# Kernel tuning notes

Measured on AMD Instinct MI355X. Metric: run time of the kernel, lower is better.

## Reference

```python
import jax, jax.numpy as jnp
import numpy as np

BATCH, IN_DIM, H, OUT_DIM = 131072, 1024, 256, 256


def _het_act(z, act_id):
    # Per-column heterogeneous activation: act_id[j] in {0:relu,1:tanh,2:gelu(exact),3:sigmoid}
    return jnp.select(
        [act_id == 0, act_id == 1, act_id == 2],
        [jax.nn.relu(z), jnp.tanh(z), jax.nn.gelu(z, approximate=False)],
        jax.nn.sigmoid(z),
    )


def setup_inputs() -> dict:
    key = jax.random.key(0)
    ks = jax.random.split(key, 7)
    def lin(k, fan_in, fan_out):
        bound = 1.0 / np.sqrt(fan_in)
        kw, kb = jax.random.split(k)
        W = jax.random.uniform(kw, (fan_in, fan_out), jnp.float32, -bound, bound)
        b = jax.random.uniform(kb, (fan_out,), jnp.float32, -bound, bound)
        return W, b
    x = jax.random.normal(ks[0], (BATCH, IN_DIM), jnp.float32)
    W1, b1 = lin(ks[1], IN_DIM, H)
    W2, b2 = lin(ks[2], H, H)
    Wout, bout = lin(ks[3], H, OUT_DIM)
    act_id1 = jnp.arange(H, dtype=jnp.int32) % 4  # relu,tanh,gelu,sigmoid cycle
    act_id2 = jnp.arange(H, dtype=jnp.int32) % 4
    return {"x": x, "W1": W1, "b1": b1, "W2": W2, "b2": b2,
            "Wout": Wout, "bout": bout, "act_id1": act_id1, "act_id2": act_id2}


def reference(x, W1, b1, W2, b2, Wout, bout, act_id1, act_id2):
    # Each original layer is 'H' separate Linear(in,1) ops concatenated -> one fused
    # [in, H] matmul with per-column activation, identical math.
    h1 = _het_act(x @ W1 + b1, act_id1)   # [B, H]
    h2 = _het_act(h1 @ W2 + b2, act_id2)  # [B, H]
    return h2 @ Wout + bout               # [B, OUT_DIM]
```

## Files before the change

### kernel.cpp

```cpp
#include <hip/hip_runtime.h>
#include <hip/hip_bf16.h>


typedef __bf16 bf16;
typedef __bf16 bf16x8 __attribute__((ext_vector_type(8)));
typedef float  f32x4  __attribute__((ext_vector_type(4)));

#define BATCH 131072
#define K1    1024
#define HDIM  256

__device__ __forceinline__ float het_act(float z, int aid) {
    if (aid == 0) return fmaxf(z, 0.0f);
    if (aid == 1) {
        float zc = fminf(fmaxf(z, -20.0f), 20.0f);
        float e = __expf(-2.0f * zc);
        return (1.0f - e) / (1.0f + e);
    }
    if (aid == 2) return 0.5f * z * (1.0f + erff(z * 0.70710678118654752f));
    return 1.0f / (1.0f + __expf(-z));
}

__global__ void prep_w(const float* __restrict__ src, bf16* __restrict__ dst,
                       int total, int kshift, int N) {
    int i = blockIdx.x * blockDim.x + threadIdx.x;
    if (i >= total) return;
    int n = i >> kshift;
    int k = i & ((1 << kshift) - 1);
    dst[i] = (bf16)src[(size_t)k * N + n];
}

#define RMA 128
#define BKA 64
#define ASTR 72
#define HSTR 264

__global__ __launch_bounds__(512, 4) void gemm1_kernel(
    const float* __restrict__ x,
    const bf16*  __restrict__ wt1,
    const float* __restrict__ b1,
    const int*   __restrict__ aid1,
    bf16* __restrict__ h1)
{
    __shared__ __align__(16) char smem[RMA * HSTR * 2];
    bf16 (*as)[ASTR] = (bf16(*)[ASTR])smem;
    bf16 (*ws)[ASTR] = (bf16(*)[ASTR])(smem + RMA * ASTR * 2);
    bf16 (*hout)[HSTR] = (bf16(*)[HSTR])smem;

    const int tid  = threadIdx.x;
    const int lane = tid & 63;
    const int wave = tid >> 6;
    const int rg   = wave >> 2;
    const int slab = wave & 3;
    const int l15  = lane & 15;
    const int quad = lane >> 4;
    const size_t row0 = (size_t)blockIdx.x * RMA;

    const int xr0 = tid >> 3;
    const int xr1 = xr0 + 64;
    const int xq  = tid & 7;
    const int wn0 = tid >> 3;
    const int wq  = tid & 7;

    f32x4 acc[4][4];
    #pragma unroll
    for (int i = 0; i < 4; ++i)
        #pragma unroll
        for (int j = 0; j < 4; ++j)
            acc[i][j] = (f32x4){0.f, 0.f, 0.f, 0.f};

    bf16x8 wcur[4], wnxt[4];
    #pragma unroll
    for (int p = 0; p < 4; ++p)
        wcur[p] = *(const bf16x8*)(wt1 + (size_t)(wn0 + p * 64) * K1 + wq * 8);

    for (int kt = 0; kt < K1 / BKA; ++kt) {
        const int k0 = kt * BKA;
        const float* xp0 = x + (row0 + xr0) * K1 + k0 + xq * 8;
        const float* xp1 = x + (row0 + xr1) * K1 + k0 + xq * 8;
        float4 f0a = *(const float4*)xp0;
        float4 f0b = *(const float4*)(xp0 + 4);
        float4 f1a = *(const float4*)xp1;
        float4 f1b = *(const float4*)(xp1 + 4);
        const int k0n = (kt + 1 < K1 / BKA) ? k0 + BKA : 0;
        #pragma unroll
        for (int p = 0; p < 4; ++p)
            wnxt[p] = *(const bf16x8*)(wt1 + (size_t)(wn0 + p * 64) * K1 + k0n + wq * 8);
        #pragma unroll
        for (int p = 0; p < 4; ++p)
            *(bf16x8*)&ws[wn0 + p * 64][wq * 8] = wcur[p];
        {
            bf16x8 va, vb;
            va[0] = (bf16)f0a.x; va[1] = (bf16)f0a.y; va[2] = (bf16)f0a.z; va[3] = (bf16)f0a.w;
            va[4] = (bf16)f0b.x; va[5] = (bf16)f0b.y; va[6] = (bf16)f0b.z; va[7] = (bf16)f0b.w;
            *(bf16x8*)&as[xr0][xq * 8] = va;
            vb[0] = (bf16)f1a.x; vb[1] = (bf16)f1a.y; vb[2] = (bf16)f1a.z; vb[3] = (bf16)f1a.w;
            vb[4] = (bf16)f1b.x; vb[5] = (bf16)f1b.y; vb[6] = (bf16)f1b.z; vb[7] = (bf16)f1b.w;
            *(bf16x8*)&as[xr1][xq * 8] = vb;
        }
        __syncthreads();
        #pragma unroll
        for (int s = 0; s < 2; ++s) {
            bf16x8 afr[4];
            #pragma unroll
            for (int i = 0; i < 4; ++i)
                afr[i] = *(const bf16x8*)&as[rg * 64 + i * 16 + l15][s * 32 + quad * 8];
            #pragma unroll
            for (int j = 0; j < 4; ++j) {
                bf16x8 bfr = *(const bf16x8*)&ws[slab * 64 + j * 16 + l15][s * 32 + quad * 8];
                #pragma unroll
                for (int i = 0; i < 4; ++i)
                    acc[i][j] = __builtin_amdgcn_mfma_f32_16x16x32_bf16(afr[i], bfr, acc[i][j], 0, 0, 0);
            }
        }
        __syncthreads();
        #pragma unroll
        for (int p = 0; p < 4; ++p) wcur[p] = wnxt[p];
    }

    #pragma unroll
    for (int j = 0; j < 4; ++j) {
        int col = slab * 64 + j * 16 + l15;
        float bias = b1[col];
        int aid = aid1[col];
        #pragma unroll
        for (int i = 0; i < 4; ++i)
            #pragma unroll
            for (int r = 0; r < 4; ++r) {
                int row = rg * 64 + i * 16 + quad * 4 + r;
                hout[row][col] = (bf16)het_act(acc[i][j][r] + bias, aid);
            }
    }
    __syncthreads();
    #pragma unroll
    for (int p = 0; p < 8; ++p) {
        int c = tid + p * 512;
        int r = c >> 5, q = c & 31;
        *(bf16x8*)(h1 + (row0 + r) * HDIM + q * 8) = *(const bf16x8*)&hout[r][q * 8];
    }
}

#define RMB 64
#define BKB 64
#define BSTR 72
#define BHSTR 264

__global__ __launch_bounds__(512, 4) void gemm23_kernel(
    const bf16*  __restrict__ h1,
    const bf16*  __restrict__ wt2,
    const float* __restrict__ b2,
    const bf16*  __restrict__ wt3,
    const float* __restrict__ bout,
    const int*   __restrict__ aid2,
    float* __restrict__ out)
{
    __shared__ __align__(16) bf16 hs[RMB][BHSTR];
    __shared__ __align__(16) bf16 ws[HDIM][BSTR];

    const int tid  = threadIdx.x;
    const int lane = tid & 63;
    const int wave = tid >> 6;
    const int rg   = wave >> 2;
    const int slab = wave & 3;
    const int l15  = lane & 15;
    const int quad = lane >> 4;
    const size_t row0 = (size_t)blockIdx.x * RMB;
    const int wn0 = tid >> 3;
    const int wq  = tid & 7;

    bf16x8 hreg[4];
    #pragma unroll
    for (int p = 0; p < 4; ++p) {
        int c = tid + p * 512;
        int r = c >> 5, q = c & 31;
        hreg[p] = *(const bf16x8*)(h1 + (row0 + r) * HDIM + q * 8);
    }
    bf16x8 wcur[4], wnxt[4];
    #pragma unroll
    for (int p = 0; p < 4; ++p)
        wcur[p] = *(const bf16x8*)(wt2 + (size_t)(wn0 + p * 64) * HDIM + wq * 8);
    #pragma unroll
    for (int p = 0; p < 4; ++p) {
        int c = tid + p * 512;
        int r = c >> 5, q = c & 31;
        *(bf16x8*)&hs[r][q * 8] = hreg[p];
    }

    f32x4 acc[2][4];

    #pragma unroll
    for (int i = 0; i < 2; ++i)
        #pragma unroll
        for (int j = 0; j < 4; ++j)
            acc[i][j] = (f32x4){0.f, 0.f, 0.f, 0.f};

    #pragma unroll
    for (int kt = 0; kt < HDIM / BKB; ++kt) {
        const int k0 = kt * BKB;
        #pragma unroll
        for (int p = 0; p < 4; ++p)
            *(bf16x8*)&ws[wn0 + p * 64][wq * 8] = wcur[p];
        const int   k0n  = (kt < 3) ? k0 + BKB : 0;
        const bf16* wsrc = (kt < 3) ? wt2 : wt3;
        #pragma unroll
        for (int p = 0; p < 4; ++p)
            wnxt[p] = *(const bf16x8*)(wsrc + (size_t)(wn0 + p * 64) * HDIM + k0n + wq * 8);
        __syncthreads();
        #pragma unroll
        for (int s = 0; s < 2; ++s) {
            bf16x8 afr[2];
            #pragma unroll
            for (int i = 0; i < 2; ++i)
                afr[i] = *(const bf16x8*)&hs[rg * 32 + i * 16 + l15][k0 + s * 32 + quad * 8];
            #pragma unroll
            for (int j = 0; j < 4; ++j) {
                bf16x8 bfr = *(const bf16x8*)&ws[slab * 64 + j * 16 + l15][s * 32 + quad * 8];
                #pragma unroll
                for (int i = 0; i < 2; ++i)
                    acc[i][j] = __builtin_amdgcn_mfma_f32_16x16x32_bf16(afr[i], bfr, acc[i][j], 0, 0, 0);
            }
        }
        __syncthreads();
        #pragma unroll
        for (int p = 0; p < 4; ++p) wcur[p] = wnxt[p];
    }
    #pragma unroll
    for (int j = 0; j < 4; ++j) {
        int col = slab * 64 + j * 16 + l15;
        float bias = b2[col];
        int aid = aid2[col];
        #pragma unroll
        for (int i = 0; i < 2; ++i)
            #pragma unroll
            for (int r = 0; r < 4; ++r) {
                int row = rg * 32 + i * 16 + quad * 4 + r;
                hs[row][col] = (bf16)het_act(acc[i][j][r] + bias, aid);
            }
    }

    #pragma unroll
    for (int i = 0; i < 2; ++i)
        #pragma unroll
        for (int j = 0; j < 4; ++j)
            acc[i][j] = (f32x4){0.f, 0.f, 0.f, 0.f};

    #pragma unroll
    for (int kt = 0; kt < HDIM / BKB; ++kt) {
        const int k0 = kt * BKB;
        #pragma unroll
        for (int p = 0; p < 4; ++p)
            *(bf16x8*)&ws[wn0 + p * 64][wq * 8] = wcur[p];
        const int k0n = (kt < 3) ? k0 + BKB : 0;
        #pragma unroll
        for (int p = 0; p < 4; ++p)
            wnxt[p] = *(const bf16x8*)(wt3 + (size_t)(wn0 + p * 64) * HDIM + k0n + wq * 8);
        __syncthreads();
        #pragma unroll
        for (int s = 0; s < 2; ++s) {
            bf16x8 afr[2];
            #pragma unroll
            for (int i = 0; i < 2; ++i)
                afr[i] = *(const bf16x8*)&hs[rg * 32 + i * 16 + l15][k0 + s * 32 + quad * 8];
            #pragma unroll
            for (int j = 0; j < 4; ++j) {
                bf16x8 bfr = *(const bf16x8*)&ws[slab * 64 + j * 16 + l15][s * 32 + quad * 8];
                #pragma unroll
                for (int i = 0; i < 2; ++i)
                    acc[i][j] = __builtin_amdgcn_mfma_f32_16x16x32_bf16(afr[i], bfr, acc[i][j], 0, 0, 0);
            }
        }
        __syncthreads();
        #pragma unroll
        for (int p = 0; p < 4; ++p) wcur[p] = wnxt[p];
    }
    #pragma unroll
    for (int j = 0; j < 4; ++j) {
        int col = slab * 64 + j * 16 + l15;
        float bias = bout[col];
        #pragma unroll
        for (int i = 0; i < 2; ++i)
            #pragma unroll
            for (int r = 0; r < 4; ++r) {
                int row = rg * 32 + i * 16 + quad * 4 + r;
                out[(row0 + row) * HDIM + col] = acc[i][j][r] + bias;
            }
    }
}

#define FRM 64
#define FAPAD 40
#define FHPAD 264

__global__ __launch_bounds__(256, 2) void hetnet_fused(
    const float* __restrict__ x, const bf16* __restrict__ wt1, const float* __restrict__ b1,
    const bf16* __restrict__ wt2, const float* __restrict__ b2,
    const bf16* __restrict__ wt3, const float* __restrict__ bout,
    const int* __restrict__ aid1, const int* __restrict__ aid2, float* __restrict__ out)
{
    __shared__ __align__(16) bf16 hs[FRM][FHPAD];
    __shared__ __align__(16) bf16 as[FRM][FAPAD];
    __shared__ __align__(16) bf16 ws[HDIM][FAPAD];

    const int tid = threadIdx.x, lane = tid & 63, wave = tid >> 6;
    const int l15 = lane & 15, quad = lane >> 4;
    const size_t row0 = (size_t)blockIdx.x * FRM;
    f32x4 acc[4][4];

    #pragma unroll
    for (int i = 0; i < 4; ++i)
        #pragma unroll
        for (int j = 0; j < 4; ++j) acc[i][j] = (f32x4){0.f,0.f,0.f,0.f};
    for (int kt = 0; kt < K1 / 32; ++kt) {
        const int k0 = kt * 32;
        { int r = tid >> 2, q = tid & 3;
          const float* xp = x + (row0 + r) * K1 + k0 + q * 8;
          float4 f0 = *(const float4*)xp; float4 f1 = *(const float4*)(xp + 4);
          bf16x8 v; v[0]=(bf16)f0.x; v[1]=(bf16)f0.y; v[2]=(bf16)f0.z; v[3]=(bf16)f0.w;
          v[4]=(bf16)f1.x; v[5]=(bf16)f1.y; v[6]=(bf16)f1.z; v[7]=(bf16)f1.w;
          *(bf16x8*)&as[r][q * 8] = v; }
        #pragma unroll
        for (int p = 0; p < 4; ++p) {
            int c = tid + p * 256, n = c >> 2, q = c & 3;
            *(bf16x8*)&ws[n][q * 8] = *(const bf16x8*)(wt1 + (size_t)n * K1 + k0 + q * 8);
        }
        __syncthreads();
        bf16x8 afr[4];
        #pragma unroll
        for (int i = 0; i < 4; ++i) afr[i] = *(const bf16x8*)&as[i*16 + l15][quad*8];
        #pragma unroll
        for (int j = 0; j < 4; ++j) {
            bf16x8 bfr = *(const bf16x8*)&ws[wave*64 + j*16 + l15][quad*8];
            #pragma unroll
            for (int i = 0; i < 4; ++i)
                acc[i][j] = __builtin_amdgcn_mfma_f32_16x16x32_bf16(afr[i], bfr, acc[i][j], 0,0,0);
        }
        __syncthreads();
    }
    #pragma unroll
    for (int j = 0; j < 4; ++j) {
        int col = wave*64 + j*16 + l15; float bias = b1[col]; int aid = aid1[col];
        #pragma unroll
        for (int i = 0; i < 4; ++i)
            #pragma unroll
            for (int r = 0; r < 4; ++r)
                hs[i*16 + quad*4 + r][col] = (bf16)het_act(acc[i][j][r] + bias, aid);
    }
    const bf16* wts[2] = {wt2, wt3};
    for (int g = 0; g < 2; ++g) {
        #pragma unroll
        for (int i = 0; i < 4; ++i)
            #pragma unroll
            for (int j = 0; j < 4; ++j) acc[i][j] = (f32x4){0.f,0.f,0.f,0.f};
        for (int kt = 0; kt < HDIM / 32; ++kt) {
            const int k0 = kt * 32;
            #pragma unroll
            for (int p = 0; p < 4; ++p) {
                int c = tid + p * 256, n = c >> 2, q = c & 3;
                *(bf16x8*)&ws[n][q * 8] = *(const bf16x8*)(wts[g] + (size_t)n * HDIM + k0 + q * 8);
            }
            __syncthreads();
            bf16x8 afr[4];
            #pragma unroll
            for (int i = 0; i < 4; ++i) afr[i] = *(const bf16x8*)&hs[i*16 + l15][k0 + quad*8];
            #pragma unroll
            for (int j = 0; j < 4; ++j) {
                bf16x8 bfr = *(const bf16x8*)&ws[wave*64 + j*16 + l15][quad*8];
                #pragma unroll
                for (int i = 0; i < 4; ++i)
                    acc[i][j] = __builtin_amdgcn_mfma_f32_16x16x32_bf16(afr[i], bfr, acc[i][j], 0,0,0);
            }
            __syncthreads();
        }
        if (g == 0) {
            #pragma unroll
            for (int j = 0; j < 4; ++j) {
                int col = wave*64 + j*16 + l15; float bias = b2[col]; int aid = aid2[col];
                #pragma unroll
                for (int i = 0; i < 4; ++i)
                    #pragma unroll
                    for (int r = 0; r < 4; ++r)
                        hs[i*16 + quad*4 + r][col] = (bf16)het_act(acc[i][j][r] + bias, aid);
            }
        } else {
            #pragma unroll
            for (int j = 0; j < 4; ++j) {
                int col = wave*64 + j*16 + l15; float bias = bout[col];
                #pragma unroll
                for (int i = 0; i < 4; ++i)
                    #pragma unroll
                    for (int r = 0; r < 4; ++r)
                        out[(row0 + i*16 + quad*4 + r) * HDIM + col] = acc[i][j][r] + bias;
            }
        }
    }
}

extern "C" void kernel_launch(void* const* d_in, const int* in_sizes, int n_in,
                              void* d_out, int out_size, void* d_ws, size_t ws_size,
                              hipStream_t stream) {
    const float* x    = (const float*)d_in[0];
    const float* W1   = (const float*)d_in[1];
    const float* b1   = (const float*)d_in[2];
    const float* W2   = (const float*)d_in[3];
    const float* b2   = (const float*)d_in[4];
    const float* Wout = (const float*)d_in[5];
    const float* bout = (const float*)d_in[6];
    const int*   aid1 = (const int*)d_in[7];
    const int*   aid2 = (const int*)d_in[8];
    float* out = (float*)d_out;

    bf16* wt1 = (bf16*)d_ws;
    bf16* wt2 = wt1 + 256 * 1024;
    bf16* wt3 = wt2 + 256 * 256;
    bf16* h1  = wt3 + 256 * 256;

    const size_t need = (size_t)(256 * 1024 + 2 * 256 * 256) * 2
                      + (size_t)BATCH * HDIM * 2;

    prep_w<<<(K1 * HDIM + 255) / 256, 256, 0, stream>>>(W1, wt1, K1 * HDIM, 10, HDIM);
    prep_w<<<(HDIM * HDIM + 255) / 256, 256, 0, stream>>>(W2, wt2, HDIM * HDIM, 8, HDIM);
    prep_w<<<(HDIM * HDIM + 255) / 256, 256, 0, stream>>>(Wout, wt3, HDIM * HDIM, 8, HDIM);

    if (ws_size >= need) {
        gemm1_kernel<<<BATCH / RMA, 512, 0, stream>>>(x, wt1, b1, aid1, h1);
        gemm23_kernel<<<BATCH / RMB, 512, 0, stream>>>(h1, wt2, b2, wt3, bout, aid2, out);
    } else {
        hetnet_fused<<<BATCH / FRM, 256, 0, stream>>>(x, wt1, b1, wt2, b2, wt3, bout,
                                                      aid1, aid2, out);
    }
}
```

Baseline: 982.2 us.

## Fuse all three layers into one kernel with B-fragments read from global

Measured after the change: 952.1 us. 3.1% less time.

```diff
diff --git a/kernel.cpp b/kernel.cpp
--- a/kernel.cpp
+++ b/kernel.cpp
@@ -30,22 +30,23 @@
     dst[i] = (bf16)src[(size_t)k * N + n];
 }
 
-#define RMA 128
-#define BKA 64
+#define RM   128
 #define ASTR 72
 #define HSTR 264
 
-__global__ __launch_bounds__(512, 4) void gemm1_kernel(
+__global__ __launch_bounds__(512, 4) void hetnet_one(
     const float* __restrict__ x,
     const bf16*  __restrict__ wt1,
-    const float* __restrict__ b1,
-    const int*   __restrict__ aid1,
-    bf16* __restrict__ h1)
+    const float* __restrict__ b1,  const int* __restrict__ aid1,
+    const bf16*  __restrict__ wt2,
+    const float* __restrict__ b2,  const int* __restrict__ aid2,
+    const bf16*  __restrict__ wt3,
+    const float* __restrict__ bout,
+    float* __restrict__ out)
 {
-    __shared__ __align__(16) char smem[RMA * HSTR * 2];
+    __shared__ __align__(16) char smem[RM * HSTR * 2];
     bf16 (*as)[ASTR] = (bf16(*)[ASTR])smem;
-    bf16 (*ws)[ASTR] = (bf16(*)[ASTR])(smem + RMA * ASTR * 2);
-    bf16 (*hout)[HSTR] = (bf16(*)[HSTR])smem;
+    bf16 (*hs)[HSTR] = (bf16(*)[HSTR])smem;
 
     const int tid  = threadIdx.x;
     const int lane = tid & 63;
@@ -54,13 +55,11 @@
     const int slab = wave & 3;
     const int l15  = lane & 15;
     const int quad = lane >> 4;
-    const size_t row0 = (size_t)blockIdx.x * RMA;
-
-    const int xr0 = tid >> 3;
-    const int xr1 = xr0 + 64;
-    const int xq  = tid & 7;
-    const int wn0 = tid >> 3;
-    const int wq  = tid & 7;
+    const size_t row0 = (size_t)blockIdx.x * RM;
+
+    const int xr = tid >> 3;
+    const int xq = tid & 7;
+    const float* xbase = x + (row0 + xr) * K1 + xq * 8;
 
     f32x4 acc[4][4];
     #pragma unroll
@@ -69,329 +68,147 @@
         for (int j = 0; j < 4; ++j)
             acc[i][j] = (f32x4){0.f, 0.f, 0.f, 0.f};
 
-    bf16x8 wcur[4], wnxt[4];
-    #pragma unroll
-    for (int p = 0; p < 4; ++p)
-        wcur[p] = *(const bf16x8*)(wt1 + (size_t)(wn0 + p * 64) * K1 + wq * 8);
-
-    for (int kt = 0; kt < K1 / BKA; ++kt) {
-        const int k0 = kt * BKA;
-        const float* xp0 = x + (row0 + xr0) * K1 + k0 + xq * 8;
-        const float* xp1 = x + (row0 + xr1) * K1 + k0 + xq * 8;
-        float4 f0a = *(const float4*)xp0;
-        float4 f0b = *(const float4*)(xp0 + 4);
-        float4 f1a = *(const float4*)xp1;
-        float4 f1b = *(const float4*)(xp1 + 4);
-        const int k0n = (kt + 1 < K1 / BKA) ? k0 + BKA : 0;
-        #pragma unroll
-        for (int p = 0; p < 4; ++p)
-            wnxt[p] = *(const bf16x8*)(wt1 + (size_t)(wn0 + p * 64) * K1 + k0n + wq * 8);
-        #pragma unroll
-        for (int p = 0; p < 4; ++p)
-            *(bf16x8*)&ws[wn0 + p * 64][wq * 8] = wcur[p];
-        {
-            bf16x8 va, vb;
-            va[0] = (bf16)f0a.x; va[1] = (bf16)f0a.y; va[2] = (bf16)f0a.z; va[3] = (bf16)f0a.w;
-            va[4] = (bf16)f0b.x; va[5] = (bf16)f0b.y; va[6] = (bf16)f0b.z; va[7] = (bf16)f0b.w;
-            *(bf16x8*)&as[xr0][xq * 8] = va;
-            vb[0] = (bf16)f1a.x; vb[1] = (bf16)f1a.y; vb[2] = (bf16)f1a.z; vb[3] = (bf16)f1a.w;
-            vb[4] = (bf16)f1b.x; vb[5] = (bf16)f1b.y; vb[6] = (bf16)f1b.z; vb[7] = (bf16)f1b.w;
-            *(bf16x8*)&as[xr1][xq * 8] = vb;
-        }
-        __syncthreads();
+    {
+        float4 f0 = *(const float4*)(xbase);
+        float4 f1 = *(const float4*)(xbase + 4);
+        float4 f2 = *(const float4*)(xbase + (size_t)64 * K1);
+        float4 f3 = *(const float4*)(xbase + (size_t)64 * K1 + 4);
+        bf16x8 va, vb;
+        va[0]=(bf16)f0.x; va[1]=(bf16)f0.y; va[2]=(bf16)f0.z; va[3]=(bf16)f0.w;
+        va[4]=(bf16)f1.x; va[5]=(bf16)f1.y; va[6]=(bf16)f1.z; va[7]=(bf16)f1.w;
+        vb[0]=(bf16)f2.x; vb[1]=(bf16)f2.y; vb[2]=(bf16)f2.z; vb[3]=(bf16)f2.w;
+        vb[4]=(bf16)f3.x; vb[5]=(bf16)f3.y; vb[6]=(bf16)f3.z; vb[7]=(bf16)f3.w;
+        *(bf16x8*)&as[xr][xq * 8] = va;
+        *(bf16x8*)&as[64 + xr][xq * 8] = vb;
+    }
+    __syncthreads();
+
+    for (int kt = 0; kt < K1 / 64; ++kt) {
+        const int buf  = (kt & 1) * RM;
+        const int nbuf = RM - buf;
+        float4 f0, f1, f2, f3;
+        if (kt < 15) {
+            const float* xp = xbase + (kt + 1) * 64;
+            f0 = *(const float4*)(xp);
+            f1 = *(const float4*)(xp + 4);
+            f2 = *(const float4*)(xp + (size_t)64 * K1);
+            f3 = *(const float4*)(xp + (size_t)64 * K1 + 4);
+        }
         #pragma unroll
         for (int s = 0; s < 2; ++s) {
             bf16x8 afr[4];
             #pragma unroll
             for (int i = 0; i < 4; ++i)
-                afr[i] = *(const bf16x8*)&as[rg * 64 + i * 16 + l15][s * 32 + quad * 8];
+                afr[i] = *(const bf16x8*)&as[buf + rg * 64 + i * 16 + l15][s * 32 + quad * 8];
             #pragma unroll
             for (int j = 0; j < 4; ++j) {
-                bf16x8 bfr = *(const bf16x8*)&ws[slab * 64 + j * 16 + l15][s * 32 + quad * 8];
+                bf16x8 bfr = *(const bf16x8*)(wt1
+                    + (size_t)(slab * 64 + j * 16 + l15) * K1 + kt * 64 + s * 32 + quad * 8);
                 #pragma unroll
                 for (int i = 0; i < 4; ++i)
                     acc[i][j] = __builtin_amdgcn_mfma_f32_16x16x32_bf16(afr[i], bfr, acc[i][j], 0, 0, 0);
             }
         }
+        if (kt < 15) {
+            bf16x8 va, vb;
+            va[0]=(bf16)f0.x; va[1]=(bf16)f0.y; va[2]=(bf16)f0.z; va[3]=(bf16)f0.w;
+            va[4]=(bf16)f1.x; va[5]=(bf16)f1.y; va[6]=(bf16)f1.z; va[7]=(bf16)f1.w;
+            vb[0]=(bf16)f2.x; vb[1]=(bf16)f2.y; vb[2]=(bf16)f2.z; vb[3]=(bf16)f2.w;
+            vb[4]=(bf16)f3.x; vb[5]=(bf16)f3.y; vb[6]=(bf16)f3.z; vb[7]=(bf16)f3.w;
+            *(bf16x8*)&as[nbuf + xr][xq * 8] = va;
+            *(bf16x8*)&as[nbuf + 64 + xr][xq * 8] = vb;
+        }
         __syncthreads();
-        #pragma unroll
-        for (int p = 0; p < 4; ++p) wcur[p] = wnxt[p];
     }
 
     #pragma unroll
     for (int j = 0; j < 4; ++j) {
-        int col = slab * 64 + j * 16 + l15;
-        float bias = b1[col];
-        int aid = aid1[col];
+        const int col = slab * 64 + j * 16 + l15;
+        const float bias = b1[col];
+        const int aid = aid1[col];
         #pragma unroll
         for (int i = 0; i < 4; ++i)
             #pragma unroll
-            for (int r = 0; r < 4; ++r) {
-                int row = rg * 64 + i * 16 + quad * 4 + r;
-                hout[row][col] = (bf16)het_act(acc[i][j][r] + bias, aid);
-            }
-    }
-    __syncthreads();
-    #pragma unroll
-    for (int p = 0; p < 8; ++p) {
-        int c = tid + p * 512;
-        int r = c >> 5, q = c & 31;
-        *(bf16x8*)(h1 + (row0 + r) * HDIM + q * 8) = *(const bf16x8*)&hout[r][q * 8];
-    }
-}
-
-#define RMB 64
-#define BKB 64
-#define BSTR 72
-#define BHSTR 264
-
-__global__ __launch_bounds__(512, 4) void gemm23_kernel(
-    const bf16*  __restrict__ h1,
-    const bf16*  __restrict__ wt2,
-    const float* __restrict__ b2,
-    const bf16*  __restrict__ wt3,
-    const float* __restrict__ bout,
-    const int*   __restrict__ aid2,
-    float* __restrict__ out)
-{
-    __shared__ __align__(16) bf16 hs[RMB][BHSTR];
-    __shared__ __align__(16) bf16 ws[HDIM][BSTR];
-
-    const int tid  = threadIdx.x;
-    const int lane = tid & 63;
-    const int wave = tid >> 6;
-    const int rg   = wave >> 2;
-    const int slab = wave & 3;
-    const int l15  = lane & 15;
-    const int quad = lane >> 4;
-    const size_t row0 = (size_t)blockIdx.x * RMB;
-    const int wn0 = tid >> 3;
-    const int wq  = tid & 7;
-
-    bf16x8 hreg[4];
-    #pragma unroll
-    for (int p = 0; p < 4; ++p) {
-        int c = tid + p * 512;
-        int r = c >> 5, q = c & 31;
-        hreg[p] = *(const bf16x8*)(h1 + (row0 + r) * HDIM + q * 8);
-    }
-    bf16x8 wcur[4], wnxt[4];
-    #pragma unroll
-    for (int p = 0; p < 4; ++p)
-        wcur[p] = *(const bf16x8*)(wt2 + (size_t)(wn0 + p * 64) * HDIM + wq * 8);
-    #pragma unroll
-    for (int p = 0; p < 4; ++p) {
-        int c = tid + p * 512;
-        int r = c >> 5, q = c & 31;
-        *(bf16x8*)&hs[r][q * 8] = hreg[p];
-    }
-
-    f32x4 acc[2][4];
-
-    #pragma unroll
-    for (int i = 0; i < 2; ++i)
+            for (int r = 0; r < 4; ++r)
+                hs[rg * 64 + i * 16 + quad * 4 + r][col] = (bf16)het_act(acc[i][j][r] + bias, aid);
+    }
+    __syncthreads();
+
+    #pragma unroll
+    for (int i = 0; i < 4; ++i)
         #pragma unroll
         for (int j = 0; j < 4; ++j)
             acc[i][j] = (f32x4){0.f, 0.f, 0.f, 0.f};
 
     #pragma unroll
-    for (int kt = 0; kt < HDIM / BKB; ++kt) {
-        const int k0 = kt * BKB;
-        #pragma unroll
-        for (int p = 0; p < 4; ++p)
-            *(bf16x8*)&ws[wn0 + p * 64][wq * 8] = wcur[p];
-        const int   k0n  = (kt < 3) ? k0 + BKB : 0;
-        const bf16* wsrc = (kt < 3) ? wt2 : wt3;
-        #pragma unroll
-        for (int p = 0; p < 4; ++p)
-            wnxt[p] = *(const bf16x8*)(wsrc + (size_t)(wn0 + p * 64) * HDIM + k0n + wq * 8);
-        __syncthreads();
+    for (int kt = 0; kt < HDIM / 64; ++kt) {
         #pragma unroll
         for (int s = 0; s < 2; ++s) {
-            bf16x8 afr[2];
-            #pragma unroll
-            for (int i = 0; i < 2; ++i)
-                afr[i] = *(const bf16x8*)&hs[rg * 32 + i * 16 + l15][k0 + s * 32 + quad * 8];
+            bf16x8 afr[4];
+            #pragma unroll
+            for (int i = 0; i < 4; ++i)
+                afr[i] = *(const bf16x8*)&hs[rg * 64 + i * 16 + l15][kt * 64 + s * 32 + quad * 8];
             #pragma unroll
             for (int j = 0; j < 4; ++j) {
-                bf16x8 bfr = *(const bf16x8*)&ws[slab * 64 + j * 16 + l15][s * 32 + quad * 8];
+                bf16x8 bfr = *(const bf16x8*)(wt2
+                    + (size_t)(slab * 64 + j * 16 + l15) * HDIM + kt * 64 + s * 32 + quad * 8);
                 #pragma unroll
-                for (int i = 0; i < 2; ++i)
+                for (int i = 0; i < 4; ++i)
                     acc[i][j] = __builtin_amdgcn_mfma_f32_16x16x32_bf16(afr[i], bfr, acc[i][j], 0, 0, 0);
             }
         }
-        __syncthreads();
-        #pragma unroll
-        for (int p = 0; p < 4; ++p) wcur[p] = wnxt[p];
-    }
+    }
+    __syncthreads();
+
     #pragma unroll
     for (int j = 0; j < 4; ++j) {
-        int col = slab * 64 + j * 16 + l15;
-        float bias = b2[col];
-        int aid = aid2[col];
-        #pragma unroll
-        for (int i = 0; i < 2; ++i)
-            #pragma unroll
-            for (int r = 0; r < 4; ++r) {
-                int row = rg * 32 + i * 16 + quad * 4 + r;
-                hs[row][col] = (bf16)het_act(acc[i][j][r] + bias, aid);
-            }
-    }
-
-    #pragma unroll
-    for (int i = 0; i < 2; ++i)
+        const int col = slab * 64 + j * 16 + l15;
+        const float bias = b2[col];
+        const int aid = aid2[col];
+        #pragma unroll
+        for (int i = 0; i < 4; ++i)
+            #pragma unroll
+            for (int r = 0; r < 4; ++r)
+                hs[rg * 64 + i * 16 + quad * 4 + r][col] = (bf16)het_act(acc[i][j][r] + bias, aid);
+    }
+    __syncthreads();
+
+    #pragma unroll
+    for (int i = 0; i < 4; ++i)
         #pragma unroll
         for (int j = 0; j < 4; ++j)
             acc[i][j] = (f32x4){0.f, 0.f, 0.f, 0.f};
 
     #pragma unroll
-    for (int kt = 0; kt < HDIM / BKB; ++kt) {
-        const int k0 = kt * BKB;
-        #pragma unroll
-        for (int p = 0; p < 4; ++p)
-            *(bf16x8*)&ws[wn0 + p * 64][wq * 8] = wcur[p];
-        const int k0n = (kt < 3) ? k0 + BKB : 0;
-        #pragma unroll
-        for (int p = 0; p < 4; ++p)
-            wnxt[p] = *(const bf16x8*)(wt3 + (size_t)(wn0 + p * 64) * HDIM + k0n + wq * 8);
-        __syncthreads();
+    for (int kt = 0; kt < HDIM / 64; ++kt) {
         #pragma unroll
         for (int s = 0; s < 2; ++s) {
-            bf16x8 afr[2];
-            #pragma unroll
-            for (int i = 0; i < 2; ++i)
-                afr[i] = *(const bf16x8*)&hs[rg * 32 + i * 16 + l15][k0 + s * 32 + quad * 8];
+            bf16x8 afr[4];
+            #pragma unroll
+            for (int i = 0; i < 4; ++i)
+                afr[i] = *(const bf16x8*)&hs[rg * 64 + i * 16 + l15][kt * 64 + s * 32 + quad * 8];
             #pragma unroll
             for (int j = 0; j < 4; ++j) {
-                bf16x8 bfr = *(const bf16x8*)&ws[slab * 64 + j * 16 + l15][s * 32 + quad * 8];
-                #pragma unroll
-                for (int i = 0; i < 2; ++i)
-                    acc[i][j] = __builtin_amdgcn_mfma_f32_16x16x32_bf16(afr[i], bfr, acc[i][j], 0, 0, 0);
-            }
-        }
-        __syncthreads();
-        #pragma unroll
-        for (int p = 0; p < 4; ++p) wcur[p] = wnxt[p];
-    }
-    #pragma unroll
-    for (int j = 0; j < 4; ++j) {
-        int col = slab * 64 + j * 16 + l15;
-        float bias = bout[col];
-        #pragma unroll
-        for (int i = 0; i < 2; ++i)
-            #pragma unroll
-            for (int r = 0; r < 4; ++r) {
-                int row = rg * 32 + i * 16 + quad * 4 + r;
-                out[(row0 + row) * HDIM + col] = acc[i][j][r] + bias;
-            }
-    }
-}
-
-#define FRM 64
-#define FAPAD 40
-#define FHPAD 264
-
-__global__ __launch_bounds__(256, 2) void hetnet_fused(
-    const float* __restrict__ x, const bf16* __restrict__ wt1, const float* __restrict__ b1,
-    const bf16* __restrict__ wt2, const float* __restrict__ b2,
-    const bf16* __restrict__ wt3, const float* __restrict__ bout,
-    const int* __restrict__ aid1, const int* __restrict__ aid2, float* __restrict__ out)
-{
-    __shared__ __align__(16) bf16 hs[FRM][FHPAD];
-    __shared__ __align__(16) bf16 as[FRM][FAPAD];
-    __shared__ __align__(16) bf16 ws[HDIM][FAPAD];
-
-    const int tid = threadIdx.x, lane = tid & 63, wave = tid >> 6;
-    const int l15 = lane & 15, quad = lane >> 4;
-    const size_t row0 = (size_t)blockIdx.x * FRM;
-    f32x4 acc[4][4];
-
-    #pragma unroll
-    for (int i = 0; i < 4; ++i)
-        #pragma unroll
-        for (int j = 0; j < 4; ++j) acc[i][j] = (f32x4){0.f,0.f,0.f,0.f};
-    for (int kt = 0; kt < K1 / 32; ++kt) {
-        const int k0 = kt * 32;
-        { int r = tid >> 2, q = tid & 3;
-          const float* xp = x + (row0 + r) * K1 + k0 + q * 8;
-          float4 f0 = *(const float4*)xp; float4 f1 = *(const float4*)(xp + 4);
-          bf16x8 v; v[0]=(bf16)f0.x; v[1]=(bf16)f0.y; v[2]=(bf16)f0.z; v[3]=(bf16)f0.w;
-          v[4]=(bf16)f1.x; v[5]=(bf16)f1.y; v[6]=(bf16)f1.z; v[7]=(bf16)f1.w;
-          *(bf16x8*)&as[r][q * 8] = v; }
-        #pragma unroll
-        for (int p = 0; p < 4; ++p) {
-            int c = tid + p * 256, n = c >> 2, q = c & 3;
-            *(bf16x8*)&ws[n][q * 8] = *(const bf16x8*)(wt1 + (size_t)n * K1 + k0 + q * 8);
-        }
-        __syncthreads();
-        bf16x8 afr[4];
-        #pragma unroll
-        for (int i = 0; i < 4; ++i) afr[i] = *(const bf16x8*)&as[i*16 + l15][quad*8];
-        #pragma unroll
-        for (int j = 0; j < 4; ++j) {
-            bf16x8 bfr = *(const bf16x8*)&ws[wave*64 + j*16 + l15][quad*8];
-            #pragma unroll
-            for (int i = 0; i < 4; ++i)
-                acc[i][j] = __builtin_amdgcn_mfma_f32_16x16x32_bf16(afr[i], bfr, acc[i][j], 0,0,0);
-        }
-        __syncthreads();
-    }
-    #pragma unroll
-    for (int j = 0; j < 4; ++j) {
-        int col = wave*64 + j*16 + l15; float bias = b1[col]; int aid = aid1[col];
-        #pragma unroll
-        for (int i = 0; i < 4; ++i)
-            #pragma unroll
-            for (int r = 0; r < 4; ++r)
-                hs[i*16 + quad*4 + r][col] = (bf16)het_act(acc[i][j][r] + bias, aid);
-    }
-    const bf16* wts[2] = {wt2, wt3};
-    for (int g = 0; g < 2; ++g) {
-        #pragma unroll
-        for (int i = 0; i < 4; ++i)
-            #pragma unroll
-            for (int j = 0; j < 4; ++j) acc[i][j] = (f32x4){0.f,0.f,0.f,0.f};
-        for (int kt = 0; kt < HDIM / 32; ++kt) {
-            const int k0 = kt * 32;
-            #pragma unroll
-            for (int p = 0; p < 4; ++p) {
-                int c = tid + p * 256, n = c >> 2, q = c & 3;
-                *(bf16x8*)&ws[n][q * 8] = *(const bf16x8*)(wts[g] + (size_t)n * HDIM + k0 + q * 8);
-            }
-            __syncthreads();
-            bf16x8 afr[4];
-            #pragma unroll
-            for (int i = 0; i < 4; ++i) afr[i] = *(const bf16x8*)&hs[i*16 + l15][k0 + quad*8];
-            #pragma unroll
-            for (int j = 0; j < 4; ++j) {
-                bf16x8 bfr = *(const bf16x8*)&ws[wave*64 + j*16 + l15][quad*8];
+                bf16x8 bfr = *(const bf16x8*)(wt3
+                    + (size_t)(slab * 64 + j * 16 + l15) * HDIM + kt * 64 + s * 32 + quad * 8);
                 #pragma unroll
                 for (int i = 0; i < 4; ++i)
-                    acc[i][j] = __builtin_amdgcn_mfma_f32_16x16x32_bf16(afr[i], bfr, acc[i][j], 0,0,0);
-            }
-            __syncthreads();
-        }
-        if (g == 0) {
-            #pragma unroll
-            for (int j = 0; j < 4; ++j) {
-                int col = wave*64 + j*16 + l15; float bias = b2[col]; int aid = aid2[col];
-                #pragma unroll
-                for (int i = 0; i < 4; ++i)
-                    #pragma unroll
-                    for (int r = 0; r < 4; ++r)
-                        hs[i*16 + quad*4 + r][col] = (bf16)het_act(acc[i][j][r] + bias, aid);
-            }
-        } else {
-            #pragma unroll
-            for (int j = 0; j < 4; ++j) {
-                int col = wave*64 + j*16 + l15; float bias = bout[col];
-                #pragma unroll
-                for (int i = 0; i < 4; ++i)
-                    #pragma unroll
-                    for (int r = 0; r < 4; ++r)
-                        out[(row0 + i*16 + quad*4 + r) * HDIM + col] = acc[i][j][r] + bias;
-            }
-        }
+                    acc[i][j] = __builtin_amdgcn_mfma_f32_16x16x32_bf16(afr[i], bfr, acc[i][j], 0, 0, 0);
+            }
+        }
+    }
+
+    #pragma unroll
+    for (int j = 0; j < 4; ++j) {
+        const int col = slab * 64 + j * 16 + l15;
+        const float bias = bout[col];
+        #pragma unroll
+        for (int i = 0; i < 4; ++i)
+            #pragma unroll
+            for (int r = 0; r < 4; ++r) {
+                const int row = rg * 64 + i * 16 + quad * 4 + r;
+                out[(row0 + row) * HDIM + col] = acc[i][j][r] + bias;
+            }
     }
 }
 
@@ -412,20 +229,11 @@
     bf16* wt1 = (bf16*)d_ws;
     bf16* wt2 = wt1 + 256 * 1024;
     bf16* wt3 = wt2 + 256 * 256;
-    bf16* h1  = wt3 + 256 * 256;
-
-    const size_t need = (size_t)(256 * 1024 + 2 * 256 * 256) * 2
-                      + (size_t)BATCH * HDIM * 2;
 
     prep_w<<<(K1 * HDIM + 255) / 256, 256, 0, stream>>>(W1, wt1, K1 * HDIM, 10, HDIM);
     prep_w<<<(HDIM * HDIM + 255) / 256, 256, 0, stream>>>(W2, wt2, HDIM * HDIM, 8, HDIM);
     prep_w<<<(HDIM * HDIM + 255) / 256, 256, 0, stream>>>(Wout, wt3, HDIM * HDIM, 8, HDIM);
 
-    if (ws_size >= need) {
-        gemm1_kernel<<<BATCH / RMA, 512, 0, stream>>>(x, wt1, b1, aid1, h1);
-        gemm23_kernel<<<BATCH / RMB, 512, 0, stream>>>(h1, wt2, b2, wt3, bout, aid2, out);
-    } else {
-        hetnet_fused<<<BATCH / FRM, 256, 0, stream>>>(x, wt1, b1, wt2, b2, wt3, bout,
-                                                      aid1, aid2, out);
-    }
-}
+    hetnet_one<<<BATCH / RM, 512, 0, stream>>>(x, wt1, b1, aid1, wt2, b2, aid2,
+                                               wt3, bout, out);
+}
```
